# Kernel tuning notes

Hardware: AMD Instinct MI355X
Metric: run time of the kernel (lower is better)

The kernel has to match this reference:

```python
import jax, jax.numpy as jnp
import numpy as np

B_OUT, N, L, C = 8, 128, 32, 64
H, F, OUT = 128, 32, 1


def setup_inputs() -> dict:
    key = jax.random.key(0)
    ks = jax.random.split(key, 12)
    stdv = 1.0 / np.sqrt(H)
    u = lambda k, shape: jax.random.uniform(k, shape, jnp.float32, -stdv, stdv)
    return {
        "x": jax.random.normal(ks[0], (B_OUT, N, L, C), jnp.float32),
        "Q": u(ks[1], (H, C)),            # mogrify: ht @ Q -> (B, C)
        "R": u(ks[2], (C, H)),            # mogrify: xt @ R -> (B, H)
        "Wi": u(ks[3], (C + H, H)), "bi": jnp.zeros((H,), jnp.float32),
        "Wg": u(ks[4], (C + H, H)), "bg": jnp.zeros((H,), jnp.float32),
        "Wste": u(ks[5], (C + H, H)), "bste": jnp.zeros((H,), jnp.float32),
        "Wfre": u(ks[6], (C + H, F)), "bfre": jnp.zeros((F,), jnp.float32),
        "Wom": u(ks[7], (C + H, F)), "bom": jnp.zeros((F,), jnp.float32),
        "Wo": u(ks[8], (C + 2 * H, H)), "bo": jnp.zeros((H,), jnp.float32),
        "Wa": u(ks[9], (F, 1)), "ba": jnp.zeros((1,), jnp.float32),
        "Wout": u(ks[10], (H, OUT)), "bout": jnp.zeros((OUT,), jnp.float32),
    }


def reference(x, Q, R, Wi, bi, Wg, bg, Wste, bste, Wfre, bfre, Wom, bom, Wo, bo, Wa, ba, Wout, bout):
    b = x.shape[0]
    xs = x.reshape(-1, x.shape[-2], x.shape[-1])      # (B, L, C), B = b*N
    B = xs.shape[0]
    sig, tanh = jax.nn.sigmoid, jnp.tanh
    two_pi = 2.0 * jnp.pi

    h0 = jnp.zeros((B, H), jnp.float32)
    re0 = jnp.zeros((B, H, F), jnp.float32)
    im0 = jnp.zeros((B, H, F), jnp.float32)

    def step(carry, xt):
        h, re_s, im_s = carry
        # mogrify, 5 iterations (odd: update x, even: update h)
        xt = 2.0 * sig(h @ Q) * xt
        h = 2.0 * sig(xt @ R) * h
        xt = 2.0 * sig(h @ Q) * xt
        h = 2.0 * sig(xt @ R) * h
        xt = 2.0 * sig(h @ Q) * xt

        ih = jnp.concatenate([xt, h], axis=-1)        # (B, C+H)
        omega = two_pi * sig(ih @ Wom + bom)          # (B, F)
        i_t = sig(ih @ Wi + bi)                       # (B, H)
        c_hat = sig(ih @ Wg + bg)                     # (B, H)
        f_ste = sig(ih @ Wste + bste)                 # (B, H)
        f_fre = sig(ih @ Wfre + bfre)                 # (B, F)

        f_t = f_ste[:, :, None] * f_fre[:, None, :]   # (B, H, F) outer-product forget gate
        ic = (i_t * c_hat)[:, :, None]                # (B, H, 1)
        re_s = f_t * re_s + ic * jnp.cos(omega)[:, None, :]
        im_s = f_t * im_s + ic * jnp.sin(omega)[:, None, :]

        a_t = jnp.sqrt(re_s ** 2 + im_s ** 2)          # (B, H, F) amplitude
        c_t = tanh((a_t @ Wa + ba).squeeze(-1))        # (B, H)

        oh = jnp.concatenate([xt, h, c_t], axis=-1)   # (B, C+2H)
        o_t = sig(oh @ Wo + bo)
        h = o_t * tanh(c_t)
        return (h, re_s, im_s), None

    (h_last, _, _), _ = jax.lax.scan(step, (h0, re0, im0), jnp.swapaxes(xs, 0, 1))
    out = (h_last @ Wout + bout).squeeze()            # (B,) since OUT == 1
    return out.reshape(b, -1)
```

## Files before the change

kernel.cpp:

```cpp
#include <hip/hip_runtime.h>
#include <math.h>

namespace {
constexpr int LSEQ = 32;
constexpr int CDIM = 64;
constexpr int HDIM = 128;
constexpr int FDIM = 32;
constexpr float TWO_PI = 6.28318530717958647692f;

__device__ __forceinline__ float sigf(float x) { return 1.0f / (1.0f + __expf(-x)); }
__device__ __forceinline__ float tanh_fast(float x) { return 1.0f - 2.0f / (__expf(2.0f * x) + 1.0f); }
}

__global__ __launch_bounds__(512, 1)
void sfm_lstm_s4w8(const float* __restrict__ x,
                   const float* __restrict__ Q, const float* __restrict__ R,
                   const float* __restrict__ Wi, const float* __restrict__ bi,
                   const float* __restrict__ Wg, const float* __restrict__ bg,
                   const float* __restrict__ Wste, const float* __restrict__ bste,
                   const float* __restrict__ Wfre, const float* __restrict__ bfre,
                   const float* __restrict__ Wom, const float* __restrict__ bom,
                   const float* __restrict__ Wo, const float* __restrict__ bo,
                   const float* __restrict__ Wa, const float* __restrict__ ba,
                   const float* __restrict__ Wout, const float* __restrict__ bout,
                   float* __restrict__ out)
{
    const int t = threadIdx.x;
    const int blk = blockIdx.x;

    __shared__ float sQ[HDIM * CDIM];
    __shared__ float sR[CDIM * HDIM];
    __shared__ __align__(16) float sx[CDIM][4];
    __shared__ __align__(16) float sh[HDIM][4];
    __shared__ __align__(16) float sct[HDIM][4];
    __shared__ float sit[4][HDIM];
    __shared__ float schat[4][HDIM];
    __shared__ float sfste[4][HDIM];
    __shared__ float sffre[4][FDIM];
    __shared__ float scosv[4][FDIM];
    __shared__ float ssinv[4][FDIM];
    __shared__ __align__(16) float spart[2048];
    __shared__ float swa[FDIM];

    #pragma unroll
    for (int i = 0; i < 16; ++i) sQ[t + 512 * i] = Q[t + 512 * i];
    #pragma unroll
    for (int i = 0; i < 16; ++i) sR[t + 512 * i] = R[t + 512 * i];
    if (t < FDIM) swa[t] = Wa[t];
    sh[t >> 2][t & 3] = 0.0f;

    const int r7 = t & 127;
    const int sA = t >> 7;
    float re[FDIM], im[FDIM];
    #pragma unroll
    for (int f = 0; f < FDIM; ++f) { re[f] = 0.0f; im[f] = 0.0f; }

    const float* wG = nullptr; const float* bG = nullptr;
    int strG = HDIM, gcol = 0, reg = -1;
    if      (t < 128) { wG = Wi;   bG = bi;   strG = HDIM; gcol = t;       reg = 0; }
    else if (t < 256) { wG = Wg;   bG = bg;   strG = HDIM; gcol = t - 128; reg = 1; }
    else if (t < 384) { wG = Wste; bG = bste; strG = HDIM; gcol = t - 256; reg = 2; }
    else if (t < 416) { wG = Wfre; bG = bfre; strG = FDIM; gcol = t - 384; reg = 3; }
    else if (t < 448) { wG = Wom;  bG = bom;  strG = FDIM; gcol = t - 416; reg = 4; }
    const float gb = (reg >= 0) ? bG[gcol] : 0.0f;
    const float* wGp0 = (reg >= 0) ? (wG + gcol) : Wi;

    const float ba0 = ba[0];
    const float bor = bo[t >> 2];
    const float* xp = x + (size_t)((blk * 4 + (t >> 6)) * LSEQ) * CDIM + (t & 63);

    const int ocol = t & 127, oks = t >> 7;
    const float* woP = Wo + ocol;

    for (int ts = 0; ts < LSEQ; ++ts) {
        if (t < 256) sx[t & 63][t >> 6] = xp[ts * CDIM];
        __syncthreads();

        #pragma unroll
        for (int m = 0; m < 5; ++m) {
            if ((m & 1) == 0) {
                const int c = t & 63, k0 = (t >> 6) * 16;
                float a0 = 0.f, a1 = 0.f, a2 = 0.f, a3 = 0.f;
                #pragma unroll
                for (int kk = 0; kk < 16; ++kk) {
                    const int k = k0 + kk;
                    const float qv = sQ[k * CDIM + c];
                    const float4 h4 = *(const float4*)&sh[k][0];
                    a0 += qv * h4.x; a1 += qv * h4.y; a2 += qv * h4.z; a3 += qv * h4.w;
                }
                *(float4*)&spart[(t >> 6) * 256 + c * 4] = make_float4(a0, a1, a2, a3);
                __syncthreads();
                if (t < 256) {
                    float v = 0.f;
                    #pragma unroll
                    for (int i = 0; i < 8; ++i) v += spart[i * 256 + t];
                    sx[t >> 2][t & 3] = 2.0f * sigf(v) * sx[t >> 2][t & 3];
                }
                __syncthreads();
            } else {
                const int j = t & 127, k0 = (t >> 7) * 16;
                float a0 = 0.f, a1 = 0.f, a2 = 0.f, a3 = 0.f;
                #pragma unroll
                for (int kk = 0; kk < 16; ++kk) {
                    const int k = k0 + kk;
                    const float rv = sR[k * HDIM + j];
                    const float4 x4 = *(const float4*)&sx[k][0];
                    a0 += rv * x4.x; a1 += rv * x4.y; a2 += rv * x4.z; a3 += rv * x4.w;
                }
                *(float4*)&spart[(t >> 7) * 512 + j * 4] = make_float4(a0, a1, a2, a3);
                __syncthreads();
                {
                    const float v = spart[t] + spart[512 + t] + spart[1024 + t] + spart[1536 + t];
                    sh[t >> 2][t & 3] = 2.0f * sigf(v) * sh[t >> 2][t & 3];
                }
                __syncthreads();
            }
        }

        if (reg >= 0) {
            float g0 = 0.f, g1 = 0.f, g2 = 0.f, g3 = 0.f;
            const float* wp = wGp0;
            #pragma unroll 8
            for (int k = 0; k < CDIM; ++k) {
                const float w = *wp; wp += strG;
                const float4 i4 = *(const float4*)&sx[k][0];
                g0 += w * i4.x; g1 += w * i4.y; g2 += w * i4.z; g3 += w * i4.w;
            }
            #pragma unroll 8
            for (int k = 0; k < HDIM; ++k) {
                const float w = *wp; wp += strG;
                const float4 i4 = *(const float4*)&sh[k][0];
                g0 += w * i4.x; g1 += w * i4.y; g2 += w * i4.z; g3 += w * i4.w;
            }
            g0 += gb; g1 += gb; g2 += gb; g3 += gb;
            if (reg == 4) {
                const float o0 = TWO_PI * sigf(g0), o1 = TWO_PI * sigf(g1);
                const float o2 = TWO_PI * sigf(g2), o3 = TWO_PI * sigf(g3);
                scosv[0][gcol] = __cosf(o0); ssinv[0][gcol] = __sinf(o0);
                scosv[1][gcol] = __cosf(o1); ssinv[1][gcol] = __sinf(o1);
                scosv[2][gcol] = __cosf(o2); ssinv[2][gcol] = __sinf(o2);
                scosv[3][gcol] = __cosf(o3); ssinv[3][gcol] = __sinf(o3);
            } else {
                float* d = (reg == 0) ? &sit[0][0] : (reg == 1) ? &schat[0][0]
                         : (reg == 2) ? &sfste[0][0] : &sffre[0][0];
                const int dstr = (reg == 3) ? FDIM : HDIM;
                d[0 * dstr + gcol] = sigf(g0);
                d[1 * dstr + gcol] = sigf(g1);
                d[2 * dstr + gcol] = sigf(g2);
                d[3 * dstr + gcol] = sigf(g3);
            }
        }
        __syncthreads();

        {
            const float ic = sit[sA][r7] * schat[sA][r7];
            const float fs = sfste[sA][r7];
            float acc = 0.f;
            #pragma unroll
            for (int f = 0; f < FDIM; ++f) {
                const float ft = fs * sffre[sA][f];
                const float cv = scosv[sA][f], sv = ssinv[sA][f];
                re[f] = ft * re[f] + ic * cv;
                im[f] = ft * im[f] + ic * sv;
                acc += sqrtf(re[f] * re[f] + im[f] * im[f]) * swa[f];
            }
            sct[r7][sA] = tanh_fast(acc + ba0);
        }
        __syncthreads();

        {
            float o0 = 0.f, o1 = 0.f, o2 = 0.f, o3 = 0.f;
            if (oks == 0) {
                #pragma unroll 8
                for (int k = 0; k < 64; ++k) {
                    const float w = woP[k * HDIM];
                    const float4 i4 = *(const float4*)&sx[k][0];
                    o0 += w * i4.x; o1 += w * i4.y; o2 += w * i4.z; o3 += w * i4.w;
                }
                #pragma unroll 8
                for (int k = 0; k < 16; ++k) {
                    const float w = woP[(64 + k) * HDIM];
                    const float4 i4 = *(const float4*)&sh[k][0];
                    o0 += w * i4.x; o1 += w * i4.y; o2 += w * i4.z; o3 += w * i4.w;
                }
            } else if (oks == 1) {
                #pragma unroll 8
                for (int k = 0; k < 80; ++k) {
                    const float w = woP[(80 + k) * HDIM];
                    const float4 i4 = *(const float4*)&sh[16 + k][0];
                    o0 += w * i4.x; o1 += w * i4.y; o2 += w * i4.z; o3 += w * i4.w;
                }
            } else if (oks == 2) {
                #pragma unroll 8
                for (int k = 0; k < 32; ++k) {
                    const float w = woP[(160 + k) * HDIM];
                    const float4 i4 = *(const float4*)&sh[96 + k][0];
                    o0 += w * i4.x; o1 += w * i4.y; o2 += w * i4.z; o3 += w * i4.w;
                }
                #pragma unroll 8
                for (int k = 0; k < 48; ++k) {
                    const float w = woP[(192 + k) * HDIM];
                    const float4 i4 = *(const float4*)&sct[k][0];
                    o0 += w * i4.x; o1 += w * i4.y; o2 += w * i4.z; o3 += w * i4.w;
                }
            } else {
                #pragma unroll 8
                for (int k = 0; k < 80; ++k) {
                    const float w = woP[(240 + k) * HDIM];
                    const float4 i4 = *(const float4*)&sct[48 + k][0];
                    o0 += w * i4.x; o1 += w * i4.y; o2 += w * i4.z; o3 += w * i4.w;
                }
            }
            *(float4*)&spart[oks * 512 + ocol * 4] = make_float4(o0, o1, o2, o3);
        }
        __syncthreads();
        {
            const float v = spart[t] + spart[512 + t] + spart[1024 + t] + spart[1536 + t];
            const float o = sigf(v + bor);
            sh[t >> 2][t & 3] = o * tanh_fast(sct[t >> 2][t & 3]);
        }
        __syncthreads();
    }

    if (t < 256) {
        const int w = t >> 6, l = t & 63;
        float p = sh[l][w] * Wout[l] + sh[l + 64][w] * Wout[l + 64];
        #pragma unroll
        for (int off = 32; off > 0; off >>= 1) p += __shfl_xor(p, off);
        if (l == 0) out[blk * 4 + w] = p + bout[0];
    }
}

extern "C" void kernel_launch(void* const* d_in, const int* in_sizes, int n_in,
                              void* d_out, int out_size, void* d_ws, size_t ws_size,
                              hipStream_t stream) {
    const float* x    = (const float*)d_in[0];
    const float* Q    = (const float*)d_in[1];
    const float* R    = (const float*)d_in[2];
    const float* Wi   = (const float*)d_in[3];
    const float* bi   = (const float*)d_in[4];
    const float* Wg   = (const float*)d_in[5];
    const float* bg   = (const float*)d_in[6];
    const float* Wste = (const float*)d_in[7];
    const float* bste = (const float*)d_in[8];
    const float* Wfre = (const float*)d_in[9];
    const float* bfre = (const float*)d_in[10];
    const float* Wom  = (const float*)d_in[11];
    const float* bom  = (const float*)d_in[12];
    const float* Wo   = (const float*)d_in[13];
    const float* bo   = (const float*)d_in[14];
    const float* Wa   = (const float*)d_in[15];
    const float* ba   = (const float*)d_in[16];
    const float* Wout = (const float*)d_in[17];
    const float* bout = (const float*)d_in[18];
    float* out = (float*)d_out;

    sfm_lstm_s4w8<<<dim3(256), dim3(512), 0, stream>>>(
        x, Q, R, Wi, bi, Wg, bg, Wste, bste, Wfre, bfre, Wom, bom,
        Wo, bo, Wa, ba, Wout, bout, out);
}
```

Before: 434.5 us.

## Double block to 1024 threads and split reductions across more threads

Each block now uses 1024 threads instead of 512, which halves the per-thread K range for the mogrify matvecs, the gate matvecs (split in two with a shuffle reduction) and the output matvec, and splits the complex-state recurrence over two lanes per element. x, h and c are merged into one contiguous [320][4] shared buffer so the Wo matvec becomes a uniform loop. The next timestep's x load moves into the final phase of the current step, which removes one barrier per step. In exchange there are more partial sums to reduce and register pressure rises at 1024 threads per block, and gate weights are still read from global memory on every step.

```diff
diff --git a/kernel.cpp b/kernel.cpp
--- a/kernel.cpp
+++ b/kernel.cpp
@@ -12,80 +12,79 @@
 __device__ __forceinline__ float tanh_fast(float x) { return 1.0f - 2.0f / (__expf(2.0f * x) + 1.0f); }
 }
 
-__global__ __launch_bounds__(512, 1)
-void sfm_lstm_s4w8(const float* __restrict__ x,
-                   const float* __restrict__ Q, const float* __restrict__ R,
-                   const float* __restrict__ Wi, const float* __restrict__ bi,
-                   const float* __restrict__ Wg, const float* __restrict__ bg,
-                   const float* __restrict__ Wste, const float* __restrict__ bste,
-                   const float* __restrict__ Wfre, const float* __restrict__ bfre,
-                   const float* __restrict__ Wom, const float* __restrict__ bom,
-                   const float* __restrict__ Wo, const float* __restrict__ bo,
-                   const float* __restrict__ Wa, const float* __restrict__ ba,
-                   const float* __restrict__ Wout, const float* __restrict__ bout,
-                   float* __restrict__ out)
+__global__ __launch_bounds__(1024, 4)
+void sfm_lstm_s4w16(const float* __restrict__ x,
+                    const float* __restrict__ Q, const float* __restrict__ R,
+                    const float* __restrict__ Wi, const float* __restrict__ bi,
+                    const float* __restrict__ Wg, const float* __restrict__ bg,
+                    const float* __restrict__ Wste, const float* __restrict__ bste,
+                    const float* __restrict__ Wfre, const float* __restrict__ bfre,
+                    const float* __restrict__ Wom, const float* __restrict__ bom,
+                    const float* __restrict__ Wo, const float* __restrict__ bo,
+                    const float* __restrict__ Wa, const float* __restrict__ ba,
+                    const float* __restrict__ Wout, const float* __restrict__ bout,
+                    float* __restrict__ out)
 {
     const int t = threadIdx.x;
     const int blk = blockIdx.x;
 
     __shared__ float sQ[HDIM * CDIM];
     __shared__ float sR[CDIM * HDIM];
-    __shared__ __align__(16) float sx[CDIM][4];
-    __shared__ __align__(16) float sh[HDIM][4];
-    __shared__ __align__(16) float sct[HDIM][4];
-    __shared__ float sit[4][HDIM];
-    __shared__ float schat[4][HDIM];
-    __shared__ float sfste[4][HDIM];
-    __shared__ float sffre[4][FDIM];
-    __shared__ float scosv[4][FDIM];
-    __shared__ float ssinv[4][FDIM];
-    __shared__ __align__(16) float spart[2048];
+    __shared__ __align__(16) float soh[320][4];
+    __shared__ __align__(16) float sit[HDIM][4];
+    __shared__ __align__(16) float schat[HDIM][4];
+    __shared__ __align__(16) float sfste[HDIM][4];
+    __shared__ __align__(16) float sffre[FDIM][4];
+    __shared__ __align__(16) float scosv[FDIM][4];
+    __shared__ __align__(16) float ssinv[FDIM][4];
+    __shared__ __align__(16) float spart[4096];
     __shared__ float swa[FDIM];
 
     #pragma unroll
-    for (int i = 0; i < 16; ++i) sQ[t + 512 * i] = Q[t + 512 * i];
+    for (int i = 0; i < 8; ++i) sQ[t + 1024 * i] = Q[t + 1024 * i];
     #pragma unroll
-    for (int i = 0; i < 16; ++i) sR[t + 512 * i] = R[t + 512 * i];
+    for (int i = 0; i < 8; ++i) sR[t + 1024 * i] = R[t + 1024 * i];
     if (t < FDIM) swa[t] = Wa[t];
-    sh[t >> 2][t & 3] = 0.0f;
-
-    const int r7 = t & 127;
-    const int sA = t >> 7;
-    float re[FDIM], im[FDIM];
+    if (t < 512) soh[64 + (t >> 2)][t & 3] = 0.0f;
+
+    const int srow = t >> 3, sseq = (t >> 1) & 3, shalf = t & 1;
+    const int f0 = shalf * (FDIM / 2);
+    float re[FDIM / 2], im[FDIM / 2];
     #pragma unroll
-    for (int f = 0; f < FDIM; ++f) { re[f] = 0.0f; im[f] = 0.0f; }
-
+    for (int j = 0; j < FDIM / 2; ++j) { re[j] = 0.0f; im[j] = 0.0f; }
+
+    const int gcol448 = t >> 1, gks = t & 1;
     const float* wG = nullptr; const float* bG = nullptr;
     int strG = HDIM, gcol = 0, reg = -1;
-    if      (t < 128) { wG = Wi;   bG = bi;   strG = HDIM; gcol = t;       reg = 0; }
-    else if (t < 256) { wG = Wg;   bG = bg;   strG = HDIM; gcol = t - 128; reg = 1; }
-    else if (t < 384) { wG = Wste; bG = bste; strG = HDIM; gcol = t - 256; reg = 2; }
-    else if (t < 416) { wG = Wfre; bG = bfre; strG = FDIM; gcol = t - 384; reg = 3; }
-    else if (t < 448) { wG = Wom;  bG = bom;  strG = FDIM; gcol = t - 416; reg = 4; }
+    if      (gcol448 < 128) { wG = Wi;   bG = bi;   strG = HDIM; gcol = gcol448;       reg = 0; }
+    else if (gcol448 < 256) { wG = Wg;   bG = bg;   strG = HDIM; gcol = gcol448 - 128; reg = 1; }
+    else if (gcol448 < 384) { wG = Wste; bG = bste; strG = HDIM; gcol = gcol448 - 256; reg = 2; }
+    else if (gcol448 < 416) { wG = Wfre; bG = bfre; strG = FDIM; gcol = gcol448 - 384; reg = 3; }
+    else if (gcol448 < 448) { wG = Wom;  bG = bom;  strG = FDIM; gcol = gcol448 - 416; reg = 4; }
     const float gb = (reg >= 0) ? bG[gcol] : 0.0f;
-    const float* wGp0 = (reg >= 0) ? (wG + gcol) : Wi;
+    const float* wGp0 = (reg >= 0) ? (wG + gcol + gks * 96 * strG) : Wi;
 
     const float ba0 = ba[0];
-    const float bor = bo[t >> 2];
-    const float* xp = x + (size_t)((blk * 4 + (t >> 6)) * LSEQ) * CDIM + (t & 63);
+    const float bo_r = bo[t >> 2];
+    const float* xbase = x + (size_t)blk * 4 * LSEQ * CDIM;
 
     const int ocol = t & 127, oks = t >> 7;
     const float* woP = Wo + ocol;
 
+    if (t < 256) soh[t & 63][t >> 6] = xbase[((t >> 6) * LSEQ) * CDIM + (t & 63)];
+    __syncthreads();
+
     for (int ts = 0; ts < LSEQ; ++ts) {
-        if (t < 256) sx[t & 63][t >> 6] = xp[ts * CDIM];
-        __syncthreads();
-
         #pragma unroll
         for (int m = 0; m < 5; ++m) {
             if ((m & 1) == 0) {
-                const int c = t & 63, k0 = (t >> 6) * 16;
+                const int c = t & 63, k0 = (t >> 6) * 8;
                 float a0 = 0.f, a1 = 0.f, a2 = 0.f, a3 = 0.f;
                 #pragma unroll
-                for (int kk = 0; kk < 16; ++kk) {
+                for (int kk = 0; kk < 8; ++kk) {
                     const int k = k0 + kk;
                     const float qv = sQ[k * CDIM + c];
-                    const float4 h4 = *(const float4*)&sh[k][0];
+                    const float4 h4 = *(const float4*)&soh[64 + k][0];
                     a0 += qv * h4.x; a1 += qv * h4.y; a2 += qv * h4.z; a3 += qv * h4.w;
                 }
                 *(float4*)&spart[(t >> 6) * 256 + c * 4] = make_float4(a0, a1, a2, a3);
@@ -93,138 +92,108 @@
                 if (t < 256) {
                     float v = 0.f;
                     #pragma unroll
-                    for (int i = 0; i < 8; ++i) v += spart[i * 256 + t];
-                    sx[t >> 2][t & 3] = 2.0f * sigf(v) * sx[t >> 2][t & 3];
+                    for (int i = 0; i < 16; ++i) v += spart[i * 256 + t];
+                    soh[t >> 2][t & 3] = 2.0f * sigf(v) * soh[t >> 2][t & 3];
                 }
                 __syncthreads();
             } else {
-                const int j = t & 127, k0 = (t >> 7) * 16;
+                const int j = t & 127, k0 = (t >> 7) * 8;
                 float a0 = 0.f, a1 = 0.f, a2 = 0.f, a3 = 0.f;
                 #pragma unroll
-                for (int kk = 0; kk < 16; ++kk) {
+                for (int kk = 0; kk < 8; ++kk) {
                     const int k = k0 + kk;
                     const float rv = sR[k * HDIM + j];
-                    const float4 x4 = *(const float4*)&sx[k][0];
+                    const float4 x4 = *(const float4*)&soh[k][0];
                     a0 += rv * x4.x; a1 += rv * x4.y; a2 += rv * x4.z; a3 += rv * x4.w;
                 }
                 *(float4*)&spart[(t >> 7) * 512 + j * 4] = make_float4(a0, a1, a2, a3);
                 __syncthreads();
-                {
-                    const float v = spart[t] + spart[512 + t] + spart[1024 + t] + spart[1536 + t];
-                    sh[t >> 2][t & 3] = 2.0f * sigf(v) * sh[t >> 2][t & 3];
-                }
-                __syncthreads();
-            }
-        }
-
-        if (reg >= 0) {
+                if (t < 512) {
+                    float v = 0.f;
+                    #pragma unroll
+                    for (int i = 0; i < 8; ++i) v += spart[i * 512 + t];
+                    soh[64 + (t >> 2)][t & 3] = 2.0f * sigf(v) * soh[64 + (t >> 2)][t & 3];
+                }
+                __syncthreads();
+            }
+        }
+
+        if (gcol448 < 448) {
             float g0 = 0.f, g1 = 0.f, g2 = 0.f, g3 = 0.f;
             const float* wp = wGp0;
+            const int kbase = gks * 96;
             #pragma unroll 8
-            for (int k = 0; k < CDIM; ++k) {
+            for (int kk = 0; kk < 96; ++kk) {
                 const float w = *wp; wp += strG;
-                const float4 i4 = *(const float4*)&sx[k][0];
+                const float4 i4 = *(const float4*)&soh[kbase + kk][0];
                 g0 += w * i4.x; g1 += w * i4.y; g2 += w * i4.z; g3 += w * i4.w;
             }
-            #pragma unroll 8
-            for (int k = 0; k < HDIM; ++k) {
-                const float w = *wp; wp += strG;
-                const float4 i4 = *(const float4*)&sh[k][0];
-                g0 += w * i4.x; g1 += w * i4.y; g2 += w * i4.z; g3 += w * i4.w;
-            }
-            g0 += gb; g1 += gb; g2 += gb; g3 += gb;
-            if (reg == 4) {
-                const float o0 = TWO_PI * sigf(g0), o1 = TWO_PI * sigf(g1);
-                const float o2 = TWO_PI * sigf(g2), o3 = TWO_PI * sigf(g3);
-                scosv[0][gcol] = __cosf(o0); ssinv[0][gcol] = __sinf(o0);
-                scosv[1][gcol] = __cosf(o1); ssinv[1][gcol] = __sinf(o1);
-                scosv[2][gcol] = __cosf(o2); ssinv[2][gcol] = __sinf(o2);
-                scosv[3][gcol] = __cosf(o3); ssinv[3][gcol] = __sinf(o3);
-            } else {
-                float* d = (reg == 0) ? &sit[0][0] : (reg == 1) ? &schat[0][0]
-                         : (reg == 2) ? &sfste[0][0] : &sffre[0][0];
-                const int dstr = (reg == 3) ? FDIM : HDIM;
-                d[0 * dstr + gcol] = sigf(g0);
-                d[1 * dstr + gcol] = sigf(g1);
-                d[2 * dstr + gcol] = sigf(g2);
-                d[3 * dstr + gcol] = sigf(g3);
+            g0 += __shfl_xor(g0, 1); g1 += __shfl_xor(g1, 1);
+            g2 += __shfl_xor(g2, 1); g3 += __shfl_xor(g3, 1);
+            if (gks == 0) {
+                g0 += gb; g1 += gb; g2 += gb; g3 += gb;
+                if (reg == 4) {
+                    const float o0 = TWO_PI * sigf(g0), o1 = TWO_PI * sigf(g1);
+                    const float o2 = TWO_PI * sigf(g2), o3 = TWO_PI * sigf(g3);
+                    *(float4*)&scosv[gcol][0] = make_float4(__cosf(o0), __cosf(o1), __cosf(o2), __cosf(o3));
+                    *(float4*)&ssinv[gcol][0] = make_float4(__sinf(o0), __sinf(o1), __sinf(o2), __sinf(o3));
+                } else {
+                    float* d = (reg == 0) ? &sit[0][0] : (reg == 1) ? &schat[0][0]
+                             : (reg == 2) ? &sfste[0][0] : &sffre[0][0];
+                    *(float4*)&d[gcol * 4] = make_float4(sigf(g0), sigf(g1), sigf(g2), sigf(g3));
+                }
             }
         }
         __syncthreads();
 
         {
-            const float ic = sit[sA][r7] * schat[sA][r7];
-            const float fs = sfste[sA][r7];
+            const float ic = sit[srow][sseq] * schat[srow][sseq];
+            const float fs = sfste[srow][sseq];
             float acc = 0.f;
             #pragma unroll
-            for (int f = 0; f < FDIM; ++f) {
-                const float ft = fs * sffre[sA][f];
-                const float cv = scosv[sA][f], sv = ssinv[sA][f];
-                re[f] = ft * re[f] + ic * cv;
-                im[f] = ft * im[f] + ic * sv;
-                acc += sqrtf(re[f] * re[f] + im[f] * im[f]) * swa[f];
-            }
-            sct[r7][sA] = tanh_fast(acc + ba0);
+            for (int j = 0; j < FDIM / 2; ++j) {
+                const int f = f0 + j;
+                const float ft = fs * sffre[f][sseq];
+                const float cv = scosv[f][sseq], sv = ssinv[f][sseq];
+                re[j] = ft * re[j] + ic * cv;
+                im[j] = ft * im[j] + ic * sv;
+                acc += sqrtf(re[j] * re[j] + im[j] * im[j]) * swa[f];
+            }
+            acc += __shfl_xor(acc, 1);
+            if (shalf == 0) soh[192 + srow][sseq] = tanh_fast(acc + ba0);
         }
         __syncthreads();
 
         {
             float o0 = 0.f, o1 = 0.f, o2 = 0.f, o3 = 0.f;
-            if (oks == 0) {
-                #pragma unroll 8
-                for (int k = 0; k < 64; ++k) {
-                    const float w = woP[k * HDIM];
-                    const float4 i4 = *(const float4*)&sx[k][0];
-                    o0 += w * i4.x; o1 += w * i4.y; o2 += w * i4.z; o3 += w * i4.w;
-                }
-                #pragma unroll 8
-                for (int k = 0; k < 16; ++k) {
-                    const float w = woP[(64 + k) * HDIM];
-                    const float4 i4 = *(const float4*)&sh[k][0];
-                    o0 += w * i4.x; o1 += w * i4.y; o2 += w * i4.z; o3 += w * i4.w;
-                }
-            } else if (oks == 1) {
-                #pragma unroll 8
-                for (int k = 0; k < 80; ++k) {
-                    const float w = woP[(80 + k) * HDIM];
-                    const float4 i4 = *(const float4*)&sh[16 + k][0];
-                    o0 += w * i4.x; o1 += w * i4.y; o2 += w * i4.z; o3 += w * i4.w;
-                }
-            } else if (oks == 2) {
-                #pragma unroll 8
-                for (int k = 0; k < 32; ++k) {
-                    const float w = woP[(160 + k) * HDIM];
-                    const float4 i4 = *(const float4*)&sh[96 + k][0];
-                    o0 += w * i4.x; o1 += w * i4.y; o2 += w * i4.z; o3 += w * i4.w;
-                }
-                #pragma unroll 8
-                for (int k = 0; k < 48; ++k) {
-                    const float w = woP[(192 + k) * HDIM];
-                    const float4 i4 = *(const float4*)&sct[k][0];
-                    o0 += w * i4.x; o1 += w * i4.y; o2 += w * i4.z; o3 += w * i4.w;
-                }
-            } else {
-                #pragma unroll 8
-                for (int k = 0; k < 80; ++k) {
-                    const float w = woP[(240 + k) * HDIM];
-                    const float4 i4 = *(const float4*)&sct[48 + k][0];
-                    o0 += w * i4.x; o1 += w * i4.y; o2 += w * i4.z; o3 += w * i4.w;
-                }
+            const int k0 = oks * 40;
+            #pragma unroll 8
+            for (int kk = 0; kk < 40; ++kk) {
+                const int k = k0 + kk;
+                const float w = woP[k * HDIM];
+                const float4 i4 = *(const float4*)&soh[k][0];
+                o0 += w * i4.x; o1 += w * i4.y; o2 += w * i4.z; o3 += w * i4.w;
             }
             *(float4*)&spart[oks * 512 + ocol * 4] = make_float4(o0, o1, o2, o3);
         }
         __syncthreads();
-        {
-            const float v = spart[t] + spart[512 + t] + spart[1024 + t] + spart[1536 + t];
-            const float o = sigf(v + bor);
-            sh[t >> 2][t & 3] = o * tanh_fast(sct[t >> 2][t & 3]);
+
+        if (t < 512) {
+            float v = 0.f;
+            #pragma unroll
+            for (int i = 0; i < 8; ++i) v += spart[i * 512 + t];
+            const float o = sigf(v + bo_r);
+            soh[64 + (t >> 2)][t & 3] = o * tanh_fast(soh[192 + (t >> 2)][t & 3]);
+        } else if (t < 768 && ts + 1 < LSEQ) {
+            const int l = t - 512, c = l & 63, s2 = l >> 6;
+            soh[c][s2] = xbase[(s2 * LSEQ + ts + 1) * CDIM + c];
         }
         __syncthreads();
     }
 
     if (t < 256) {
         const int w = t >> 6, l = t & 63;
-        float p = sh[l][w] * Wout[l] + sh[l + 64][w] * Wout[l + 64];
+        float p = soh[64 + l][w] * Wout[l] + soh[128 + l][w] * Wout[64 + l];
         #pragma unroll
         for (int off = 32; off > 0; off >>= 1) p += __shfl_xor(p, off);
         if (l == 0) out[blk * 4 + w] = p + bout[0];
@@ -255,7 +224,7 @@
     const float* bout = (const float*)d_in[18];
     float* out = (float*)d_out;
 
-    sfm_lstm_s4w8<<<dim3(256), dim3(512), 0, stream>>>(
+    sfm_lstm_s4w16<<<dim3(256), dim3(1024), 0, stream>>>(
         x, Q, R, Wi, bi, Wg, bg, Wste, bste, Wfre, bfre, Wom, bom,
         Wo, bo, Wa, ba, Wout, bout, out);
 }
```

Result: slower. 677.4 us (+55.9%).
